# Performance work log

Measured on AMD Instinct MI355X. Metric: run time of the kernel, lower is better.

## Reference

```python
import jax, jax.numpy as jnp
import numpy as np
import math

D_MODEL = 2048
NUM_HEADS = 16
HEAD_DIM = D_MODEL // NUM_HEADS
B, QLEN, CACHE_LEN = 4, 512, 3584

def setup_inputs() -> dict:
    key = jax.random.key(0)
    ks = jax.random.split(key, 13)
    s = 0.02
    return {
        'query': jax.random.normal(ks[0], (B, QLEN, D_MODEL), jnp.float32),
        'key': jax.random.normal(ks[1], (B, QLEN, D_MODEL), jnp.float32),
        'value': jax.random.normal(ks[2], (B, QLEN, D_MODEL), jnp.float32),
        'cached_k': jax.random.normal(ks[3], (B, CACHE_LEN, D_MODEL), jnp.float32),
        'cached_v': jax.random.normal(ks[4], (B, CACHE_LEN, D_MODEL), jnp.float32),
        'wq': jax.random.normal(ks[5], (D_MODEL, D_MODEL), jnp.float32) * s,
        'bq': jnp.zeros((D_MODEL,), jnp.float32),
        'wk': jax.random.normal(ks[6], (D_MODEL, D_MODEL), jnp.float32) * s,
        'bk': jnp.zeros((D_MODEL,), jnp.float32),
        'wv': jax.random.normal(ks[7], (D_MODEL, D_MODEL), jnp.float32) * s,
        'bv': jnp.zeros((D_MODEL,), jnp.float32),
        'wo': jax.random.normal(ks[8], (D_MODEL, D_MODEL), jnp.float32) * s,
        'bo': jnp.zeros((D_MODEL,), jnp.float32),
    }

def _split_heads(x):
    b, s, _ = x.shape
    return x.reshape(b, s, NUM_HEADS, HEAD_DIM).transpose(0, 2, 1, 3)  # [b,h,s,d]

def reference(query, key, value, cached_k, cached_v, wq, bq, wk, bk, wv, bv, wo, bo):
    # projections (torch Linear: x @ W^T + b)
    Q = query @ wq.T + bq
    K_new = key @ wk.T + bk
    V_new = value @ wv.T + bv
    K = jnp.concatenate([cached_k, K_new], axis=1)  # [b, total, d_model]
    V = jnp.concatenate([cached_v, V_new], axis=1)
    seq_len = query.shape[1]
    total_len = K.shape[1]
    cache_len = total_len - seq_len
    Qh = _split_heads(Q)  # [b,h,q,d]
    Kh = _split_heads(K)  # [b,h,t,d]
    Vh = _split_heads(V)
    scale = math.sqrt(HEAD_DIM)
    scores = jnp.einsum('bhqd,bhtd->bhqt', Qh, Kh) / scale
    # causal mask with cache offset: query i attends to keys j <= cache_len + i
    q_idx = jnp.arange(seq_len)[:, None]
    k_idx = jnp.arange(total_len)[None, :]
    mask = k_idx > (q_idx + cache_len)  # True = masked
    scores = jnp.where(mask[None, None], -jnp.inf, scores)
    attn = jax.nn.softmax(scores, axis=-1)
    out = jnp.einsum('bhqt,bhtd->bhqd', attn, Vh)
    out = out.transpose(0, 2, 1, 3).reshape(query.shape[0], seq_len, D_MODEL)
    out = out @ wo.T + bo
    return out
```

## Files before the change

kernel.cpp:

```cpp
#include <hip/hip_runtime.h>

typedef _Float16 half8 __attribute__((ext_vector_type(8)));
typedef _Float16 half4v __attribute__((ext_vector_type(4)));
typedef float f32x4 __attribute__((ext_vector_type(4)));

#define NB 4
#define SQ 512
#define CL 3584
#define TT 4096
#define DM 2048
#define NH 16
#define DH 128

#define KSW(row, col) ((((row) * 128) + (col)) ^ ((((row) & 7) << 3)))
#define VSW(row, col) ((((row) * 64) + (col)) ^ ((((row) & 7) << 3)))
#define PSW(row, col) ((((row) * 64) + (col)) ^ ((((row) & 7) << 3)))

__device__ __forceinline__ void gl_lds16(const void* g, void* l) {
  __builtin_amdgcn_global_load_lds(
      (const __attribute__((address_space(1))) unsigned int*)g,
      (__attribute__((address_space(3))) unsigned int*)l, 16, 0, 0);
}

__global__ __launch_bounds__(256) void cvt_f16(
    const float* __restrict__ s0, const float* __restrict__ s1, const float* __restrict__ s2,
    _Float16* __restrict__ d0, _Float16* __restrict__ d1, _Float16* __restrict__ d2,
    int dstride)
{
  const float* s = blockIdx.y == 0 ? s0 : blockIdx.y == 1 ? s1 : s2;
  _Float16* d = blockIdx.y == 0 ? d0 : blockIdx.y == 1 ? d1 : d2;
  const int n4 = DM * DM / 4;
  for (int v = blockIdx.x * blockDim.x + threadIdx.x; v < n4;
       v += gridDim.x * blockDim.x) {
    float4 x = ((const float4*)s)[v];
    half4v h = { (_Float16)x.x, (_Float16)x.y, (_Float16)x.z, (_Float16)x.w };
    const int m = v >> 9, c = (v << 2) & 2047;
    *(half4v*)&d[(size_t)m * dstride + c] = h;
  }
}

__global__ __launch_bounds__(256) void convert_K(
    const float* __restrict__ ck, _Float16* __restrict__ K)
{
  const long long nvec = (long long)NB * CL * DM / 4;
  const int pb = CL * DM / 4;
  for (long long v = (long long)blockIdx.x * blockDim.x + threadIdx.x; v < nvec;
       v += (long long)gridDim.x * blockDim.x) {
    int b = (int)(v / pb);
    long long r = v - (long long)b * pb;
    float4 x = ((const float4*)ck)[v];
    half4v hx = { (_Float16)x.x, (_Float16)x.y, (_Float16)x.z, (_Float16)x.w };
    ((half4v*)K)[(long long)b * (TT * DM / 4) + r] = hx;
  }
}

__global__ __launch_bounds__(256) void transpose_V(
    const float* __restrict__ cv, _Float16* __restrict__ Vt)
{
  __shared__ _Float16 T[64][70];
  const int t0 = blockIdx.x * 64;
  const int dm0 = blockIdx.y * 64;
  const int b = blockIdx.z;
  const int tid = threadIdx.x;
  {
    const int tr = tid >> 2, c0 = (tid & 3) * 16;
    const float* src = cv + ((size_t)b * CL + t0 + tr) * DM + dm0 + c0;
    float4 a0 = ((const float4*)src)[0];
    float4 a1 = ((const float4*)src)[1];
    float4 a2 = ((const float4*)src)[2];
    float4 a3 = ((const float4*)src)[3];
    half8 h0 = { (_Float16)a0.x, (_Float16)a0.y, (_Float16)a0.z, (_Float16)a0.w,
                 (_Float16)a1.x, (_Float16)a1.y, (_Float16)a1.z, (_Float16)a1.w };
    half8 h1 = { (_Float16)a2.x, (_Float16)a2.y, (_Float16)a2.z, (_Float16)a2.w,
                 (_Float16)a3.x, (_Float16)a3.y, (_Float16)a3.z, (_Float16)a3.w };
    *(half8*)&T[tr][c0] = h0;
    *(half8*)&T[tr][c0 + 8] = h1;
  }
  __syncthreads();
  {
    const int dl = tid >> 2, tc = (tid & 3) * 16;
    const int h = dm0 >> 7, d = (dm0 & 127) + dl;
    half8 o0, o1;
#pragma unroll
    for (int i = 0; i < 8; ++i) o0[i] = T[tc + i][dl];
#pragma unroll
    for (int i = 0; i < 8; ++i) o1[i] = T[tc + 8 + i][dl];
    _Float16* dst = Vt + ((size_t)(b * NH + h) * DH + d) * TT + t0 + tc;
    *(half8*)dst = o0;
    *(half8*)(dst + 8) = o1;
  }
}

template<int MODE>
__global__ __launch_bounds__(512, 4) void mm16(
    const _Float16* __restrict__ A0, const _Float16* __restrict__ A1,
    const _Float16* __restrict__ A2, int astride,
    const _Float16* __restrict__ W0, const _Float16* __restrict__ W1,
    const _Float16* __restrict__ W2,
    const float* __restrict__ b0, const float* __restrict__ b1,
    const float* __restrict__ b2,
    _Float16* __restrict__ Qp, _Float16* __restrict__ Kc,
    _Float16* __restrict__ Vt, float* __restrict__ Co)
{
  __shared__ __align__(16) char smem[4 * 8192];
  char* Abuf = smem;
  char* Wbuf = smem + 2 * 8192;

  const int tid = threadIdx.x;
  const int bm = blockIdx.x, bn = blockIdx.y, z = blockIdx.z;
  const _Float16* Ain = z == 0 ? A0 : z == 1 ? A1 : A2;
  const _Float16* W   = z == 0 ? W0 : z == 1 ? W1 : W2;
  const float* bias   = z == 0 ? b0 : z == 1 ? b1 : b2;

  const int wid = tid >> 6, lane = tid & 63;
  const int wm = wid >> 2, wn = wid & 3;
  const int lr = lane & 15, lg = lane >> 4;

  f32x4 acc[4][2];
#pragma unroll
  for (int i = 0; i < 4; ++i)
#pragma unroll
    for (int j = 0; j < 2; ++j) acc[i][j] = (f32x4){0.f, 0.f, 0.f, 0.f};

  size_t aoff, woff;
  {
    const int o = wid * 1024 + lane * 16;
    const int prow = o >> 7, pb = o & 127;
    const int lb = pb ^ ((prow & 7) << 4);
    const int r = (prow << 1) | (lb >> 6), c = lb & 63;
    aoff = (size_t)(bm * 128 + r) * astride + c;
    woff = (size_t)(bn * 128 + r) * 4096 + c;
  }

  auto stage = [&](int kt, int buf) {
    gl_lds16((const char*)Ain + aoff + kt * 64, Abuf + buf * 8192 + wid * 1024);
    gl_lds16((const char*)W + woff + kt * 64, Wbuf + buf * 8192 + wid * 1024);
  };

  auto lds_addr = [](const char* base, int r, int cb) -> const char* {
    return base + ((r >> 1) << 7) + ((((r & 1) << 6) | cb) ^ (((r >> 1) & 7) << 4));
  };

  auto compute = [&](int buf) {
    const char* ab = Abuf + buf * 8192;
    const char* wb = Wbuf + buf * 8192;
    half8 af[4], bf[2];
#pragma unroll
    for (int i = 0; i < 4; ++i)
      af[i] = *(const half8*)lds_addr(ab, wm * 64 + i * 16 + lr, lg << 4);
#pragma unroll
    for (int j = 0; j < 2; ++j)
      bf[j] = *(const half8*)lds_addr(wb, wn * 32 + j * 16 + lr, lg << 4);
#pragma unroll
    for (int i = 0; i < 4; ++i)
#pragma unroll
      for (int j = 0; j < 2; ++j)
        acc[i][j] = __builtin_amdgcn_mfma_f32_16x16x32_f16(af[i], bf[j], acc[i][j], 0, 0, 0);
  };

  const int NKT = DM / 32;
  stage(0, 0);
  __syncthreads();
  for (int kt = 0; kt < NKT; ++kt) {
    if (kt + 1 < NKT) stage(kt + 1, (kt + 1) & 1);
    compute(kt & 1);
    __syncthreads();
  }

  const float qscale = 0.08838834764831845f * 1.4426950408889634f;
#pragma unroll
  for (int i = 0; i < 4; ++i) {
    const int m0 = bm * 128 + wm * 64 + i * 16 + lg * 4;
#pragma unroll
    for (int j = 0; j < 2; ++j) {
      const int gn = bn * 128 + wn * 32 + j * 16 + lr;
      const float bb = bias[gn];
      if constexpr (MODE == 1) {
#pragma unroll
        for (int r = 0; r < 4; ++r)
          Co[(size_t)(m0 + r) * DM + gn] = acc[i][j][r] + bb;
      } else {
        if (z == 0) {
#pragma unroll
          for (int r = 0; r < 4; ++r)
            Qp[(size_t)(m0 + r) * DM + gn] = (_Float16)((acc[i][j][r] + bb) * qscale);
        } else if (z == 1) {
          const int b = m0 >> 9;
#pragma unroll
          for (int r = 0; r < 4; ++r)
            Kc[((size_t)b * TT + CL + ((m0 + r) & 511)) * DM + gn] =
                (_Float16)(acc[i][j][r] + bb);
        } else {
          half4v hv;
#pragma unroll
          for (int r = 0; r < 4; ++r) hv[r] = (_Float16)(acc[i][j][r] + bb);
          const int b = m0 >> 9, t = CL + (m0 & 511);
          const int h = gn >> 7, d = gn & 127;
          *(half4v*)&Vt[((size_t)(b * NH + h) * DH + d) * TT + t] = hv;
        }
      }
    }
  }
}

__global__ __launch_bounds__(512) void attn_kernel(
    const _Float16* __restrict__ Qp, const _Float16* __restrict__ Kc,
    const _Float16* __restrict__ Vt, _Float16* __restrict__ AO)
{
  __shared__ _Float16 Ks[2][64 * 128];
  __shared__ _Float16 VTs[3][128 * 64];
  __shared__ _Float16 Ps[8][16 * 64];

  const int tid = threadIdx.x;
  const int lin = blockIdx.x;
  const int xcd = lin & 7, slot = lin >> 3;
  const int pair = xcd * 8 + (slot >> 2);
  const int qb = slot & 3;
  const int b = pair >> 4, h = pair & 15;
  const int q0 = qb * 128;

  const int wid = tid >> 6, lane = tid & 63;
  const int lr = lane & 15, lg = lane >> 4;
  const int qw = q0 + wid * 16;

  half8 qf[4];
#pragma unroll
  for (int kk = 0; kk < 4; ++kk)
    qf[kk] = *(const half8*)&Qp[(size_t)(b * SQ + qw + lr) * DM + h * DH + kk * 32 + lg * 8];

  f32x4 zero = {0.f, 0.f, 0.f, 0.f};
  f32x4 acc_t[8];
#pragma unroll
  for (int d = 0; d < 8; ++d) acc_t[d] = zero;
  float m_run = -1e30f, l_run = 0.f;

  const int nt = (CL + q0 + 128) / 64;
  const int kr = tid >> 4, kc = (tid & 15) << 3;
  const int vr = tid >> 2, vc = (tid & 3) << 3;
  const _Float16* Kbase = Kc + (size_t)b * TT * DM + h * DH;
  const _Float16* Vbase = Vt + (size_t)(b * NH + h) * DH * TT;

  uint4 kreg0, kreg1, vreg0, vreg1;
  auto gload_t = [&](int tt) {
    const int t0 = tt * 64;
    kreg0 = *(const uint4*)(Kbase + (size_t)(t0 + kr) * DM + kc);
    kreg1 = *(const uint4*)(Kbase + (size_t)(t0 + kr + 32) * DM + kc);
    vreg0 = *(const uint4*)(Vbase + (size_t)vr * TT + t0 + vc);
    vreg1 = *(const uint4*)(Vbase + (size_t)vr * TT + t0 + 32 + vc);
  };
  auto lwrite_t = [&](int kbuf, int vbuf) {
    *(uint4*)&Ks[kbuf][KSW(kr, kc)] = kreg0;
    *(uint4*)&Ks[kbuf][KSW(kr + 32, kc)] = kreg1;
    *(uint4*)&VTs[vbuf][VSW(vr, vc)] = vreg0;
    *(uint4*)&VTs[vbuf][VSW(vr, vc + 32)] = vreg1;
  };

  auto qk = [&](int kbuf, f32x4* sc) {
#pragma unroll
    for (int j = 0; j < 4; ++j) {
      sc[j] = zero;
      half8 kb[4];
#pragma unroll
      for (int kk = 0; kk < 4; ++kk)
        kb[kk] = *(const half8*)&Ks[kbuf][KSW(j * 16 + lr, kk * 32 + lg * 8)];
#pragma unroll
      for (int kk = 0; kk < 4; ++kk)
        sc[j] = __builtin_amdgcn_mfma_f32_16x16x32_f16(kb[kk], qf[kk], sc[j], 0, 0, 0);
    }
  };

  auto mask_s = [&](int t0, f32x4* sc) {
    if (t0 + 63 > CL + qw) {
#pragma unroll
      for (int j = 0; j < 4; ++j)
#pragma unroll
        for (int r = 0; r < 4; ++r)
          if (t0 + j * 16 + lg * 4 + r > CL + qw + lr) sc[j][r] = -1e30f;
    }
  };

  auto softmax_step = [&](f32x4* sp) {
    float mt = sp[0][0];
#pragma unroll
    for (int j = 0; j < 4; ++j)
#pragma unroll
      for (int r = 0; r < 4; ++r) mt = fmaxf(mt, sp[j][r]);
    mt = fmaxf(mt, __shfl_xor(mt, 16));
    mt = fmaxf(mt, __shfl_xor(mt, 32));
    if (!__all(mt <= m_run + 10.0f)) {
      const float mn = fmaxf(m_run, mt);
      const float fsc = exp2f(m_run - mn);
      m_run = mn;
      l_run *= fsc;
#pragma unroll
      for (int d = 0; d < 8; ++d)
#pragma unroll
        for (int r = 0; r < 4; ++r) acc_t[d][r] *= fsc;
    }
    float ps = 0.f;
#pragma unroll
    for (int j = 0; j < 4; ++j) {
      float p0 = exp2f(sp[j][0] - m_run);
      float p1 = exp2f(sp[j][1] - m_run);
      float p2 = exp2f(sp[j][2] - m_run);
      float p3 = exp2f(sp[j][3] - m_run);
      ps += (p0 + p1) + (p2 + p3);
      half4v hp = { (_Float16)p0, (_Float16)p1, (_Float16)p2, (_Float16)p3 };
      *(half4v*)&Ps[wid][PSW(lr, j * 16 + lg * 4)] = hp;
    }
    ps += __shfl_xor(ps, 16);
    ps += __shfl_xor(ps, 32);
    l_run += ps;
  };

  auto pv = [&](int vbuf) {
#pragma unroll
    for (int tf = 0; tf < 2; ++tf) {
      half8 pf = *(const half8*)&Ps[wid][PSW(lr, tf * 32 + lg * 8)];
#pragma unroll
      for (int d = 0; d < 8; ++d) {
        half8 vf = *(const half8*)&VTs[vbuf][VSW(d * 16 + lr, tf * 32 + lg * 8)];
        acc_t[d] = __builtin_amdgcn_mfma_f32_16x16x32_f16(vf, pf, acc_t[d], 0, 0, 0);
      }
    }
  };

  f32x4 sp[4], sc[4];

  gload_t(0);
  lwrite_t(0, 0);
  __syncthreads();
  gload_t(1);
  qk(0, sp);
  mask_s(0, sp);
  lwrite_t(1, 1);

  for (int t = 1; t < nt; ++t) {
    __syncthreads();
    if (t + 1 < nt) gload_t(t + 1);
    qk(t & 1, sc);
    softmax_step(sp);
    pv((t - 1) % 3);
    mask_s(t * 64, sc);
#pragma unroll
    for (int j = 0; j < 4; ++j) sp[j] = sc[j];
    if (t + 1 < nt) lwrite_t((t + 1) & 1, (t + 1) % 3);
  }
  softmax_step(sp);
  pv((nt - 1) % 3);

  const float inv = 1.0f / l_run;
#pragma unroll
  for (int d = 0; d < 8; ++d) {
    half4v hv;
#pragma unroll
    for (int r = 0; r < 4; ++r) hv[r] = (_Float16)(acc_t[d][r] * inv);
    *(half4v*)&AO[(size_t)(b * SQ + qw + lr) * DM + h * DH + d * 16 + lg * 4] = hv;
  }
}

extern "C" void kernel_launch(void* const* d_in, const int* in_sizes, int n_in,
                              void* d_out, int out_size, void* d_ws, size_t ws_size,
                              hipStream_t stream) {
  const float* query = (const float*)d_in[0];
  const float* key   = (const float*)d_in[1];
  const float* value = (const float*)d_in[2];
  const float* ck    = (const float*)d_in[3];
  const float* cv    = (const float*)d_in[4];
  const float* wq = (const float*)d_in[5];
  const float* bq = (const float*)d_in[6];
  const float* wk = (const float*)d_in[7];
  const float* bk = (const float*)d_in[8];
  const float* wv = (const float*)d_in[9];
  const float* bv = (const float*)d_in[10];
  const float* wo = (const float*)d_in[11];
  const float* bo = (const float*)d_in[12];

  char* ws = (char*)d_ws;
  _Float16* Kc = (_Float16*)ws;
  _Float16* Vt = (_Float16*)(ws + 67108864);
  _Float16* Qp = (_Float16*)(ws + 134217728);
  _Float16* AO = (_Float16*)(ws + 142606336);

  _Float16* wqh = Kc;
  _Float16* wkh = Kc + 8388608;
  _Float16* wvh = Kc + 16777216;
  _Float16* qh = Vt;
  _Float16* kh = Vt + 2048 * 4096;
  _Float16* vh = Vt + 4096 * 4096;
  _Float16* woh = Qp;

  cvt_f16<<<dim3(512, 3), 256, 0, stream>>>(query, key, value, qh, kh, vh, 4096);
  cvt_f16<<<dim3(512, 3), 256, 0, stream>>>(wq, wk, wv, wqh, wkh, wvh, 2048);
  mm16<0><<<dim3(16, 16, 3), 512, 0, stream>>>(
      qh, kh, vh, 8192, wqh, wkh, wvh, bq, bk, bv, Qp, Kc, Vt, nullptr);
  convert_K<<<2048, 256, 0, stream>>>(ck, Kc);
  transpose_V<<<dim3(CL / 64, DM / 64, NB), 256, 0, stream>>>(cv, Vt);
  attn_kernel<<<256, 512, 0, stream>>>(Qp, Kc, Vt, AO);
  cvt_f16<<<dim3(512, 1), 256, 0, stream>>>(wo, wo, wo, woh, woh, woh, 2048);
  mm16<1><<<dim3(16, 16, 1), 512, 0, stream>>>(
      AO, AO, AO, 4096, woh, woh, woh, bo, bo, bo, nullptr, nullptr, nullptr,
      (float*)d_out);
}
```

Before: 319.6 us.

## Split attention KV range into two parts and merge with a combine kernel

```diff
diff --git a/kernel.cpp b/kernel.cpp
--- a/kernel.cpp
+++ b/kernel.cpp
@@ -57,7 +57,7 @@
 __global__ __launch_bounds__(256) void transpose_V(
     const float* __restrict__ cv, _Float16* __restrict__ Vt)
 {
-  __shared__ _Float16 T[64][70];
+  __shared__ _Float16 T[64][72];
   const int t0 = blockIdx.x * 64;
   const int dm0 = blockIdx.y * 64;
   const int b = blockIdx.z;
@@ -203,19 +203,21 @@
   }
 }
 
-__global__ __launch_bounds__(512) void attn_kernel(
+__global__ __launch_bounds__(512, 4) void attn_kernel(
     const _Float16* __restrict__ Qp, const _Float16* __restrict__ Kc,
-    const _Float16* __restrict__ Vt, _Float16* __restrict__ AO)
+    const _Float16* __restrict__ Vt, _Float16* __restrict__ O0,
+    _Float16* __restrict__ O1, float2* __restrict__ ml)
 {
   __shared__ _Float16 Ks[2][64 * 128];
-  __shared__ _Float16 VTs[3][128 * 64];
+  __shared__ _Float16 VTs[2][128 * 64];
   __shared__ _Float16 Ps[8][16 * 64];
 
   const int tid = threadIdx.x;
   const int lin = blockIdx.x;
   const int xcd = lin & 7, slot = lin >> 3;
-  const int pair = xcd * 8 + (slot >> 2);
-  const int qb = slot & 3;
+  const int pair = xcd * 8 + (slot >> 3);
+  const int rem = slot & 7;
+  const int qb = rem >> 1, part = rem & 1;
   const int b = pair >> 4, h = pair & 15;
   const int q0 = qb * 128;
 
@@ -234,60 +236,73 @@
   for (int d = 0; d < 8; ++d) acc_t[d] = zero;
   float m_run = -1e30f, l_run = 0.f;
 
-  const int nt = (CL + q0 + 128) / 64;
-  const int kr = tid >> 4, kc = (tid & 15) << 3;
-  const int vr = tid >> 2, vc = (tid & 3) << 3;
-  const _Float16* Kbase = Kc + (size_t)b * TT * DM + h * DH;
-  const _Float16* Vbase = Vt + (size_t)(b * NH + h) * DH * TT;
+  const int nt_full = (CL + q0 + 128) / 64;
+  const int half = nt_full >> 1;
+  const int tbeg = part ? half : 0;
+  const int nt = part ? (nt_full - half) : half;
+
+  const int kr = tid >> 4, kg = tid & 15;
+  const int vrow = tid & 127, vg = (tid >> 7) << 1;
+  const int koff0 = KSW(kr, kg * 8), koff1 = KSW(kr + 32, kg * 8);
+  const int voff0 = VSW(vrow, vg * 8), voff1 = VSW(vrow, vg * 8 + 8);
+
+  const _Float16* kp0 = Kc + ((size_t)b * TT + tbeg * 64 + kr) * DM + h * DH + kg * 8;
+  const _Float16* kp1 = kp0 + 32 * DM;
+  const _Float16* vp = Vt + ((size_t)(b * NH + h) * DH + vrow) * TT + tbeg * 64 + vg * 8;
 
   uint4 kreg0, kreg1, vreg0, vreg1;
-  auto gload_t = [&](int tt) {
-    const int t0 = tt * 64;
-    kreg0 = *(const uint4*)(Kbase + (size_t)(t0 + kr) * DM + kc);
-    kreg1 = *(const uint4*)(Kbase + (size_t)(t0 + kr + 32) * DM + kc);
-    vreg0 = *(const uint4*)(Vbase + (size_t)vr * TT + t0 + vc);
-    vreg1 = *(const uint4*)(Vbase + (size_t)vr * TT + t0 + 32 + vc);
+  auto gload = [&]() {
+    kreg0 = *(const uint4*)kp0;
+    kreg1 = *(const uint4*)kp1;
+    vreg0 = *(const uint4*)vp;
+    vreg1 = *(const uint4*)(vp + 8);
+    kp0 += 64 * DM; kp1 += 64 * DM; vp += 64;
   };
-  auto lwrite_t = [&](int kbuf, int vbuf) {
-    *(uint4*)&Ks[kbuf][KSW(kr, kc)] = kreg0;
-    *(uint4*)&Ks[kbuf][KSW(kr + 32, kc)] = kreg1;
-    *(uint4*)&VTs[vbuf][VSW(vr, vc)] = vreg0;
-    *(uint4*)&VTs[vbuf][VSW(vr, vc + 32)] = vreg1;
+  auto lwrite = [&](int buf) {
+    *(uint4*)&Ks[buf][koff0] = kreg0;
+    *(uint4*)&Ks[buf][koff1] = kreg1;
+    *(uint4*)&VTs[buf][voff0] = vreg0;
+    *(uint4*)&VTs[buf][voff1] = vreg1;
   };
 
-  auto qk = [&](int kbuf, f32x4* sc) {
+  gload();
+  lwrite(0);
+
+  for (int tt = 0; tt < nt; ++tt) {
+    __syncthreads();
+    const bool more = (tt + 1 < nt);
+    if (more) gload();
+    const int cur = tt & 1;
+
+    f32x4 s[4];
 #pragma unroll
     for (int j = 0; j < 4; ++j) {
-      sc[j] = zero;
+      s[j] = zero;
       half8 kb[4];
 #pragma unroll
       for (int kk = 0; kk < 4; ++kk)
-        kb[kk] = *(const half8*)&Ks[kbuf][KSW(j * 16 + lr, kk * 32 + lg * 8)];
+        kb[kk] = *(const half8*)&Ks[cur][KSW(j * 16 + lr, kk * 32 + lg * 8)];
 #pragma unroll
       for (int kk = 0; kk < 4; ++kk)
-        sc[j] = __builtin_amdgcn_mfma_f32_16x16x32_f16(kb[kk], qf[kk], sc[j], 0, 0, 0);
-    }
-  };
-
-  auto mask_s = [&](int t0, f32x4* sc) {
+        s[j] = __builtin_amdgcn_mfma_f32_16x16x32_f16(kb[kk], qf[kk], s[j], 0, 0, 0);
+    }
+
+    const int t0 = (tbeg + tt) * 64;
     if (t0 + 63 > CL + qw) {
 #pragma unroll
       for (int j = 0; j < 4; ++j)
 #pragma unroll
         for (int r = 0; r < 4; ++r)
-          if (t0 + j * 16 + lg * 4 + r > CL + qw + lr) sc[j][r] = -1e30f;
-    }
-  };
-
-  auto softmax_step = [&](f32x4* sp) {
-    float mt = sp[0][0];
-#pragma unroll
-    for (int j = 0; j < 4; ++j)
-#pragma unroll
-      for (int r = 0; r < 4; ++r) mt = fmaxf(mt, sp[j][r]);
-    mt = fmaxf(mt, __shfl_xor(mt, 16));
-    mt = fmaxf(mt, __shfl_xor(mt, 32));
+          if (t0 + j * 16 + lg * 4 + r > CL + qw + lr) s[j][r] = -1e30f;
+    }
+
+    float mt = fmaxf(fmaxf(fmaxf(s[0][0], s[0][1]), fmaxf(s[0][2], s[0][3])),
+                     fmaxf(fmaxf(s[1][0], s[1][1]), fmaxf(s[1][2], s[1][3])));
+    mt = fmaxf(mt, fmaxf(fmaxf(fmaxf(s[2][0], s[2][1]), fmaxf(s[2][2], s[2][3])),
+                         fmaxf(fmaxf(s[3][0], s[3][1]), fmaxf(s[3][2], s[3][3]))));
     if (!__all(mt <= m_run + 10.0f)) {
+      mt = fmaxf(mt, __shfl_xor(mt, 16));
+      mt = fmaxf(mt, __shfl_xor(mt, 32));
       const float mn = fmaxf(m_run, mt);
       const float fsc = exp2f(m_run - mn);
       m_run = mn;
@@ -300,63 +315,69 @@
     float ps = 0.f;
 #pragma unroll
     for (int j = 0; j < 4; ++j) {
-      float p0 = exp2f(sp[j][0] - m_run);
-      float p1 = exp2f(sp[j][1] - m_run);
-      float p2 = exp2f(sp[j][2] - m_run);
-      float p3 = exp2f(sp[j][3] - m_run);
+      float p0 = exp2f(s[j][0] - m_run);
+      float p1 = exp2f(s[j][1] - m_run);
+      float p2 = exp2f(s[j][2] - m_run);
+      float p3 = exp2f(s[j][3] - m_run);
       ps += (p0 + p1) + (p2 + p3);
       half4v hp = { (_Float16)p0, (_Float16)p1, (_Float16)p2, (_Float16)p3 };
       *(half4v*)&Ps[wid][PSW(lr, j * 16 + lg * 4)] = hp;
     }
-    ps += __shfl_xor(ps, 16);
-    ps += __shfl_xor(ps, 32);
     l_run += ps;
-  };
-
-  auto pv = [&](int vbuf) {
+
 #pragma unroll
     for (int tf = 0; tf < 2; ++tf) {
       half8 pf = *(const half8*)&Ps[wid][PSW(lr, tf * 32 + lg * 8)];
 #pragma unroll
       for (int d = 0; d < 8; ++d) {
-        half8 vf = *(const half8*)&VTs[vbuf][VSW(d * 16 + lr, tf * 32 + lg * 8)];
+        half8 vf = *(const half8*)&VTs[cur][VSW(d * 16 + lr, tf * 32 + lg * 8)];
         acc_t[d] = __builtin_amdgcn_mfma_f32_16x16x32_f16(vf, pf, acc_t[d], 0, 0, 0);
       }
     }
-  };
-
-  f32x4 sp[4], sc[4];
-
-  gload_t(0);
-  lwrite_t(0, 0);
-  __syncthreads();
-  gload_t(1);
-  qk(0, sp);
-  mask_s(0, sp);
-  lwrite_t(1, 1);
-
-  for (int t = 1; t < nt; ++t) {
-    __syncthreads();
-    if (t + 1 < nt) gload_t(t + 1);
-    qk(t & 1, sc);
-    softmax_step(sp);
-    pv((t - 1) % 3);
-    mask_s(t * 64, sc);
-#pragma unroll
-    for (int j = 0; j < 4; ++j) sp[j] = sc[j];
-    if (t + 1 < nt) lwrite_t((t + 1) & 1, (t + 1) % 3);
-  }
-  softmax_step(sp);
-  pv((nt - 1) % 3);
-
-  const float inv = 1.0f / l_run;
+
+    if (more) lwrite(cur ^ 1);
+  }
+
+  float lt = l_run + __shfl_xor(l_run, 16);
+  lt += __shfl_xor(lt, 32);
+  const float inv = 1.0f / lt;
+  _Float16* Od = part ? O1 : O0;
 #pragma unroll
   for (int d = 0; d < 8; ++d) {
     half4v hv;
 #pragma unroll
     for (int r = 0; r < 4; ++r) hv[r] = (_Float16)(acc_t[d][r] * inv);
-    *(half4v*)&AO[(size_t)(b * SQ + qw + lr) * DM + h * DH + d * 16 + lg * 4] = hv;
-  }
+    *(half4v*)&Od[(size_t)(b * SQ + qw + lr) * DM + h * DH + d * 16 + lg * 4] = hv;
+  }
+  if (lg == 0) {
+    float2 e; e.x = m_run; e.y = lt;
+    ml[part * (64 * SQ) + ((b * NH + h) * SQ) + qw + lr] = e;
+  }
+}
+
+__global__ __launch_bounds__(256) void combine(
+    _Float16* __restrict__ AO, const _Float16* __restrict__ O1,
+    const float2* __restrict__ ml)
+{
+  const int idx = blockIdx.x * 256 + threadIdx.x;
+  const int row = idx >> 8;
+  const int col0 = (idx & 255) * 8;
+  const int b = row >> 9, q = row & 511, h = col0 >> 7;
+  const float2 e0 = ml[(b * NH + h) * SQ + q];
+  const float2 e1 = ml[64 * SQ + (b * NH + h) * SQ + q];
+  const float m = fmaxf(e0.x, e1.x);
+  float w0 = e0.y * exp2f(e0.x - m);
+  float w1 = e1.y * exp2f(e1.x - m);
+  const float inv = 1.0f / (w0 + w1);
+  w0 *= inv; w1 *= inv;
+  const size_t o = (size_t)row * DM + col0;
+  half8 a = *(const half8*)&AO[o];
+  half8 c = *(const half8*)&O1[o];
+  half8 r;
+#pragma unroll
+  for (int i = 0; i < 8; ++i)
+    r[i] = (_Float16)(w0 * (float)a[i] + w1 * (float)c[i]);
+  *(half8*)&AO[o] = r;
 }
 
 extern "C" void kernel_launch(void* const* d_in, const int* in_sizes, int n_in,
@@ -382,6 +403,9 @@
   _Float16* Qp = (_Float16*)(ws + 134217728);
   _Float16* AO = (_Float16*)(ws + 142606336);
 
+  _Float16* O1s = (_Float16*)d_out;
+  float2* mls = (float2*)((char*)d_out + 8388608);
+
   _Float16* wqh = Kc;
   _Float16* wkh = Kc + 8388608;
   _Float16* wvh = Kc + 16777216;
@@ -396,7 +420,8 @@
       qh, kh, vh, 8192, wqh, wkh, wvh, bq, bk, bv, Qp, Kc, Vt, nullptr);
   convert_K<<<2048, 256, 0, stream>>>(ck, Kc);
   transpose_V<<<dim3(CL / 64, DM / 64, NB), 256, 0, stream>>>(cv, Vt);
-  attn_kernel<<<256, 512, 0, stream>>>(Qp, Kc, Vt, AO);
+  attn_kernel<<<512, 512, 0, stream>>>(Qp, Kc, Vt, AO, O1s, mls);
+  combine<<<2048, 256, 0, stream>>>(AO, O1s, mls);
   cvt_f16<<<dim3(512, 1), 256, 0, stream>>>(wo, wo, wo, woh, woh, woh, 2048);
   mm16<1><<<dim3(16, 16, 1), 512, 0, stream>>>(
       AO, AO, AO, 4096, woh, woh, woh, bo, bo, bo, nullptr, nullptr, nullptr,
```

Measured after the change: 461.6 us. 1.44x slower.
